# Performance work log

Hardware: AMD Instinct MI355X
Metric: run time of the kernel (lower is better)

Reference implementation:

```python
import jax, jax.numpy as jnp
import numpy as np
from jax import lax

# 4D convolution via lax.conv_general_dilated (supports N spatial dims natively)
# Layout: x is (N, C, T, U, V, W); weight is (O, I, kT, kU, kV, kW)

def conv4d(x, w, b):
    dn = lax.conv_dimension_numbers(x.shape, w.shape, ('NCTUVW', 'OITUVW', 'NCTUVW'))
    y = lax.conv_general_dilated(x, w, window_strides=(1, 1, 1, 1), padding='SAME',
                                 dimension_numbers=dn)
    return y + b[None, :, None, None, None, None]


def setup_inputs() -> dict:
    key = jax.random.key(0)
    k0, k1, k2, k3, k4 = jax.random.split(key, 5)
    B, C_in, C_hid, C_out = 2, 64, 128, 64
    T, D, H, W = 4, 16, 32, 32
    K = 3  # kernel size per dim (stmode 'C' -> (3,3,3,3))
    x = jax.random.normal(k0, (B, C_in, T, D, H, W), dtype=jnp.float32)
    scale1 = 1.0 / np.sqrt(C_in * K ** 4)
    scale2 = 1.0 / np.sqrt(C_hid * K ** 4)
    w1 = jax.random.normal(k1, (C_hid, C_in, K, K, K, K), dtype=jnp.float32) * scale1
    b1 = jax.random.normal(k2, (C_hid,), dtype=jnp.float32) * scale1
    w2 = jax.random.normal(k3, (C_out, C_hid, K, K, K, K), dtype=jnp.float32) * scale2
    b2 = jax.random.normal(k4, (C_out,), dtype=jnp.float32) * scale2
    return {"x": x, "w1": w1, "b1": b1, "w2": w2, "b2": b2}


def reference(x, w1, b1, w2, b2):
    # conv1 -> ReLU -> (dropout p=0 is identity) -> conv2 -> (dropout identity)
    h = jax.nn.relu(conv4d(x, w1, b1))
    return conv4d(h, w2, b2)
```

## Files before the change

kernel.cpp:

```cpp
#include <hip/hip_runtime.h>


using bf16x8 = __attribute__((ext_vector_type(8))) __bf16;
using f32x16 = __attribute__((ext_vector_type(16))) float;
using f32x4  = __attribute__((ext_vector_type(4))) float;

__global__ __launch_bounds__(256) void cvt_x(const float* __restrict__ x,
                                             __bf16* __restrict__ x_t) {
    __shared__ float lt[64][65];
    const int nb = blockIdx.y;
    const int p0 = blockIdx.x * 64;
    const float* src = x + (size_t)nb * 64 * 65536;
    __bf16* dst = x_t + (size_t)nb * 65536 * 64;
    #pragma unroll
    for (int i = 0; i < 16; ++i) {
        int idx = i * 256 + threadIdx.x;
        int c = idx >> 6, p = idx & 63;
        lt[c][p] = src[(size_t)c * 65536 + p0 + p];
    }
    __syncthreads();
    #pragma unroll
    for (int i = 0; i < 16; ++i) {
        int idx = i * 256 + threadIdx.x;
        int p = idx >> 6, c = idx & 63;
        dst[(size_t)(p0 + p) * 64 + c] = (__bf16)lt[c][p];
    }
}

template <int CIN>
__global__ __launch_bounds__(256) void cvt_w(const float* __restrict__ w,
                                             __bf16* __restrict__ wt) {
    constexpr int LOG = (CIN == 64) ? 6 : 7;
    constexpr int COUT = 8192 / CIN;
    int oc = blockIdx.x * 256 + threadIdx.x;
    if (oc >= 8192) return;
    const int o = oc >> LOG, c = oc & (CIN - 1);
    const int kg = c >> 4, cl = c & 15;
    const float* src = w + (size_t)oc * 81;
    #pragma unroll 1
    for (int tap = 0; tap < 81; ++tap)
        wt[(((size_t)tap * (CIN / 16) + kg) * COUT + o) * 16 + cl] = (__bf16)src[tap];
}

template <int CIN, int COUT, int MT, int NT, int CHALVES, bool RELU>
__global__ __launch_bounds__(256, 2) void conv4d_mfma(
    const __bf16* __restrict__ in_t,
    const __bf16* __restrict__ wt,
    const float* __restrict__ bias,
    __bf16* __restrict__ out_bf,
    float* __restrict__ out_f)
{
    __shared__ uint4 tile4[340 * 8];

    const int tid  = threadIdx.x;
    const int lane = tid & 63;
    const int l31  = lane & 31;
    const int hl   = lane >> 5;
    const int wv   = tid >> 6;
    const int gmi  = wv >> 1;
    const int gni  = wv & 1;

    const int bid = blockIdx.x;
    const int vg = bid & 3;
    const int u  = (bid >> 2) & 15;
    const int t  = (bid >> 6) & 3;
    const int nb = bid >> 8;
    const int v0 = vg * 8;
    const int pbase = ((t * 16 + u) * 32 + v0) * 32;

    const __bf16* inb = in_t + (size_t)nb * 65536 * CIN;

    f32x16 acc[MT][NT];
    #pragma unroll
    for (int mt = 0; mt < MT; ++mt)
        #pragma unroll
        for (int nt = 0; nt < NT; ++nt)
            #pragma unroll
            for (int i = 0; i < 16; ++i)
                acc[mt][nt][i] = 0.f;

    #pragma unroll 1
    for (int kt = 0; kt < 3; ++kt) {
        const int t_in = t + kt - 1;
        if ((unsigned)t_in >= 4u) continue;
        #pragma unroll 1
        for (int ku = 0; ku < 3; ++ku) {
            const int u_in = u + ku - 1;
            if ((unsigned)u_in >= 16u) continue;
            const int rowbase = (t_in * 16 + u_in) * 1024;
            #pragma unroll 1
            for (int ch = 0; ch < CHALVES; ++ch) {
                __syncthreads();
                #pragma unroll 1
                for (int idx = tid; idx < 2720; idx += 256) {
                    const int c = idx & 7, pos = idx >> 3;
                    const int r = pos / 34, wp = pos - r * 34;
                    const int v_in = v0 - 1 + r, w_in = wp - 1;
                    uint4 val = make_uint4(0u, 0u, 0u, 0u);
                    if (((unsigned)v_in < 32u) && ((unsigned)w_in < 32u))
                        val = *(const uint4*)(inb +
                              (size_t)(rowbase + v_in * 32 + w_in) * CIN +
                              ch * 64 + c * 8);
                    tile4[pos * 8 + (c ^ (pos & 7))] = val;
                }
                __syncthreads();
                const int tap00 = (kt * 3 + ku) * 3;
                #pragma unroll 1
                for (int kv = 0; kv < 3; ++kv) {
                    #pragma unroll
                    for (int kw = 0; kw < 3; ++kw) {
                        const int tap = (tap00 + kv) * 3 + kw;
                        const __bf16* bbase = wt +
                            ((size_t)tap * (CIN / 16) + ch * 4) * (COUT * 16);
                        #pragma unroll
                        for (int ks = 0; ks < 4; ++ks) {
                            bf16x8 af[MT];
                            #pragma unroll
                            for (int mt = 0; mt < MT; ++mt) {
                                const int pos = (gmi * MT + mt + kv) * 34 + l31 + kw;
                                af[mt] = *(const bf16x8*)&tile4[pos * 8 +
                                         ((ks * 2 + hl) ^ (pos & 7))];
                            }
                            bf16x8 bfv[NT];
                            #pragma unroll
                            for (int nt = 0; nt < NT; ++nt) {
                                const int o = (gni * NT + nt) * 32 + l31;
                                bfv[nt] = *(const bf16x8*)(bbase +
                                          (size_t)ks * (COUT * 16) + o * 16 + hl * 8);
                            }
                            #pragma unroll
                            for (int mt = 0; mt < MT; ++mt)
                                #pragma unroll
                                for (int nt = 0; nt < NT; ++nt)
                                    acc[mt][nt] = __builtin_amdgcn_mfma_f32_32x32x16_bf16(
                                        af[mt], bfv[nt], acc[mt][nt], 0, 0, 0);
                        }
                    }
                }
            }
        }
    }

    #pragma unroll
    for (int nt = 0; nt < NT; ++nt) {
        const int o = (gni * NT + nt) * 32 + l31;
        const float bv = bias[o];
        #pragma unroll
        for (int mt = 0; mt < MT; ++mt) {
            const int pb = pbase + (gmi * MT + mt) * 32;
            if constexpr (RELU) {
                #pragma unroll
                for (int rg = 0; rg < 4; ++rg)
                    #pragma unroll
                    for (int j = 0; j < 4; ++j) {
                        float v = acc[mt][nt][rg * 4 + j] + bv;
                        v = v > 0.f ? v : 0.f;
                        const int p = pb + j + 8 * rg + 4 * hl;
                        out_bf[(size_t)(nb * 65536 + p) * COUT + o] = (__bf16)v;
                    }
            } else {
                #pragma unroll
                for (int rg = 0; rg < 4; ++rg) {
                    f32x4 s;
                    #pragma unroll
                    for (int j = 0; j < 4; ++j)
                        s[j] = acc[mt][nt][rg * 4 + j] + bv;
                    const int p = pb + 8 * rg + 4 * hl;
                    *(f32x4*)(out_f + ((size_t)nb * COUT + o) * 65536 + p) = s;
                }
            }
        }
    }
}

extern "C" void kernel_launch(void* const* d_in, const int* in_sizes, int n_in,
                              void* d_out, int out_size, void* d_ws, size_t ws_size,
                              hipStream_t stream) {
    const float* x  = (const float*)d_in[0];
    const float* w1 = (const float*)d_in[1];
    const float* b1 = (const float*)d_in[2];
    const float* w2 = (const float*)d_in[3];
    const float* b2 = (const float*)d_in[4];
    float* out = (float*)d_out;

    char* ws = (char*)d_ws;
    __bf16* x_t = (__bf16*)ws;
    __bf16* h_t = (__bf16*)(ws + 16777216);
    __bf16* w1t = (__bf16*)(ws + 16777216 + 33554432);
    __bf16* w2t = (__bf16*)(ws + 16777216 + 33554432 + 1327104);

    cvt_x<<<dim3(1024, 2), 256, 0, stream>>>(x, x_t);
    cvt_w<64><<<32, 256, 0, stream>>>(w1, w1t);
    cvt_w<128><<<32, 256, 0, stream>>>(w2, w2t);

    conv4d_mfma<64, 128, 4, 2, 1, true><<<512, 256, 0, stream>>>(x_t, w1t, b1, h_t, nullptr);
    conv4d_mfma<128, 64, 4, 1, 2, false><<<512, 256, 0, stream>>>(h_t, w2t, b2, nullptr, out);
}
```

Measured before the change: 456.2 us.

## Stage input tiles with direct global-to-LDS loads and reuse A fragments across kv

```diff
diff --git a/kernel.cpp b/kernel.cpp
--- a/kernel.cpp
+++ b/kernel.cpp
@@ -4,6 +4,12 @@
 using bf16x8 = __attribute__((ext_vector_type(8))) __bf16;
 using f32x16 = __attribute__((ext_vector_type(16))) float;
 using f32x4  = __attribute__((ext_vector_type(4))) float;
+
+typedef __attribute__((address_space(1))) const void as1_void;
+typedef __attribute__((address_space(3))) void as3_void;
+__device__ __forceinline__ void gload_lds16(const void* g, void* l) {
+    __builtin_amdgcn_global_load_lds((as1_void*)g, (as3_void*)l, 16, 0, 0);
+}
 
 __global__ __launch_bounds__(256) void cvt_x(const float* __restrict__ x,
                                              __bf16* __restrict__ x_t) {
@@ -42,15 +48,17 @@
         wt[(((size_t)tap * (CIN / 16) + kg) * COUT + o) * 16 + cl] = (__bf16)src[tap];
 }
 
-template <int CIN, int COUT, int MT, int NT, int CHALVES, bool RELU>
+template <int CIN, int COUT, int NT, int CHALVES, bool RELU>
 __global__ __launch_bounds__(256, 2) void conv4d_mfma(
     const __bf16* __restrict__ in_t,
     const __bf16* __restrict__ wt,
     const float* __restrict__ bias,
     __bf16* __restrict__ out_bf,
-    float* __restrict__ out_f)
+    float* __restrict__ out_f,
+    const __bf16* __restrict__ zp)
 {
-    __shared__ uint4 tile4[340 * 8];
+    constexpr int KST = CIN / 16;
+    __shared__ __bf16 tile[3072 * 8];
 
     const int tid  = threadIdx.x;
     const int lane = tid & 63;
@@ -61,18 +69,45 @@
     const int gni  = wv & 1;
 
     const int bid = blockIdx.x;
-    const int vg = bid & 3;
-    const int u  = (bid >> 2) & 15;
-    const int t  = (bid >> 6) & 3;
-    const int nb = bid >> 8;
-    const int v0 = vg * 8;
+    const int xcd = bid & 7;
+    const int s   = bid >> 3;
+    const int u   = xcd * 2 + (s & 1);
+    const int vg  = (s >> 1) & 3;
+    const int t   = (s >> 3) & 3;
+    const int nb  = (s >> 5) & 1;
+    const int v0  = vg * 8;
     const int pbase = ((t * 16 + u) * 32 + v0) * 32;
 
     const __bf16* inb = in_t + (size_t)nb * 65536 * CIN;
 
-    f32x16 acc[MT][NT];
-    #pragma unroll
-    for (int mt = 0; mt < MT; ++mt)
+    int goff[12];
+    #pragma unroll
+    for (int it = 0; it < 12; ++it) {
+        const int idx = it * 256 + tid;
+        const int row = idx / 272;
+        const int rem = idx - row * 272;
+        const int chunk = rem / 34;
+        const int wp  = rem - chunk * 34;
+        const int v_in = v0 - 1 + row;
+        const int w_in = wp - 1;
+        const bool ok = (row < 10) && ((unsigned)v_in < 32u) && ((unsigned)w_in < 32u);
+        goff[it] = ok ? ((v_in * 32 + w_in) * CIN + chunk * 8) : -1;
+    }
+
+    const bf16x8* tile16 = (const bf16x8*)tile;
+    const bf16x8* abase[3];
+    #pragma unroll
+    for (int kw = 0; kw < 3; ++kw)
+        abase[kw] = tile16 + (gmi * 1088 + hl * 34 + l31 + kw);
+
+    const __bf16* wlane[NT];
+    #pragma unroll
+    for (int nt = 0; nt < NT; ++nt)
+        wlane[nt] = wt + ((gni * NT + nt) * 32 + l31) * 16 + hl * 8;
+
+    f32x16 acc[4][NT];
+    #pragma unroll
+    for (int mt = 0; mt < 4; ++mt)
         #pragma unroll
         for (int nt = 0; nt < NT; ++nt)
             #pragma unroll
@@ -87,55 +122,48 @@
         for (int ku = 0; ku < 3; ++ku) {
             const int u_in = u + ku - 1;
             if ((unsigned)u_in >= 16u) continue;
-            const int rowbase = (t_in * 16 + u_in) * 1024;
+            const int tapbase = (kt * 3 + ku) * 9;
+            const __bf16* gstage0 = inb + (size_t)((t_in * 16 + u_in) * 1024) * CIN;
             #pragma unroll 1
             for (int ch = 0; ch < CHALVES; ++ch) {
+                const __bf16* gstage = gstage0 + ch * 64;
                 __syncthreads();
-                #pragma unroll 1
-                for (int idx = tid; idx < 2720; idx += 256) {
-                    const int c = idx & 7, pos = idx >> 3;
-                    const int r = pos / 34, wp = pos - r * 34;
-                    const int v_in = v0 - 1 + r, w_in = wp - 1;
-                    uint4 val = make_uint4(0u, 0u, 0u, 0u);
-                    if (((unsigned)v_in < 32u) && ((unsigned)w_in < 32u))
-                        val = *(const uint4*)(inb +
-                              (size_t)(rowbase + v_in * 32 + w_in) * CIN +
-                              ch * 64 + c * 8);
-                    tile4[pos * 8 + (c ^ (pos & 7))] = val;
+                #pragma unroll
+                for (int it = 0; it < 12; ++it) {
+                    const __bf16* gp = (goff[it] >= 0) ? (gstage + goff[it]) : zp;
+                    char* lp = ((char*)tile) + it * 4096 + wv * 1024;
+                    gload_lds16(gp, lp);
                 }
                 __syncthreads();
-                const int tap00 = (kt * 3 + ku) * 3;
-                #pragma unroll 1
-                for (int kv = 0; kv < 3; ++kv) {
-                    #pragma unroll
-                    for (int kw = 0; kw < 3; ++kw) {
-                        const int tap = (tap00 + kv) * 3 + kw;
-                        const __bf16* bbase = wt +
-                            ((size_t)tap * (CIN / 16) + ch * 4) * (COUT * 16);
+                #pragma unroll
+                for (int ks = 0; ks < 4; ++ks) {
+                    const int ksg = ch * 4 + ks;
+                    bf16x8 af[6][3];
+                    #pragma unroll
+                    for (int r = 0; r < 6; ++r)
                         #pragma unroll
-                        for (int ks = 0; ks < 4; ++ks) {
-                            bf16x8 af[MT];
+                        for (int kw = 0; kw < 3; ++kw)
+                            af[r][kw] = abase[kw][r * 272 + ks * 68];
+                    #pragma unroll
+                    for (int kv = 0; kv < 3; ++kv)
+                        #pragma unroll
+                        for (int kw = 0; kw < 3; ++kw) {
+                            const size_t wo =
+                                ((size_t)(tapbase + kv * 3 + kw) * KST + ksg) *
+                                (COUT * 16);
+                            bf16x8 bv[NT];
                             #pragma unroll
-                            for (int mt = 0; mt < MT; ++mt) {
-                                const int pos = (gmi * MT + mt + kv) * 34 + l31 + kw;
-                                af[mt] = *(const bf16x8*)&tile4[pos * 8 +
-                                         ((ks * 2 + hl) ^ (pos & 7))];
-                            }
-                            bf16x8 bfv[NT];
+                            for (int nt = 0; nt < NT; ++nt)
+                                bv[nt] = *(const bf16x8*)(wlane[nt] + wo);
                             #pragma unroll
-                            for (int nt = 0; nt < NT; ++nt) {
-                                const int o = (gni * NT + nt) * 32 + l31;
-                                bfv[nt] = *(const bf16x8*)(bbase +
-                                          (size_t)ks * (COUT * 16) + o * 16 + hl * 8);
-                            }
-                            #pragma unroll
-                            for (int mt = 0; mt < MT; ++mt)
+                            for (int r = kv; r < kv + 4; ++r)
                                 #pragma unroll
                                 for (int nt = 0; nt < NT; ++nt)
-                                    acc[mt][nt] = __builtin_amdgcn_mfma_f32_32x32x16_bf16(
-                                        af[mt], bfv[nt], acc[mt][nt], 0, 0, 0);
+                                    acc[r - kv][nt] =
+                                        __builtin_amdgcn_mfma_f32_32x32x16_bf16(
+                                            af[r][kw], bv[nt], acc[r - kv][nt],
+                                            0, 0, 0);
                         }
-                    }
                 }
             }
         }
@@ -146,8 +174,8 @@
         const int o = (gni * NT + nt) * 32 + l31;
         const float bv = bias[o];
         #pragma unroll
-        for (int mt = 0; mt < MT; ++mt) {
-            const int pb = pbase + (gmi * MT + mt) * 32;
+        for (int mt = 0; mt < 4; ++mt) {
+            const int pb = pbase + (gmi * 4 + mt) * 32;
             if constexpr (RELU) {
                 #pragma unroll
                 for (int rg = 0; rg < 4; ++rg)
@@ -161,12 +189,12 @@
             } else {
                 #pragma unroll
                 for (int rg = 0; rg < 4; ++rg) {
-                    f32x4 s;
+                    f32x4 sv;
                     #pragma unroll
                     for (int j = 0; j < 4; ++j)
-                        s[j] = acc[mt][nt][rg * 4 + j] + bv;
+                        sv[j] = acc[mt][nt][rg * 4 + j] + bv;
                     const int p = pb + 8 * rg + 4 * hl;
-                    *(f32x4*)(out_f + ((size_t)nb * COUT + o) * 65536 + p) = s;
+                    *(f32x4*)(out_f + ((size_t)nb * COUT + o) * 65536 + p) = sv;
                 }
             }
         }
@@ -186,13 +214,17 @@
     char* ws = (char*)d_ws;
     __bf16* x_t = (__bf16*)ws;
     __bf16* h_t = (__bf16*)(ws + 16777216);
-    __bf16* w1t = (__bf16*)(ws + 16777216 + 33554432);
-    __bf16* w2t = (__bf16*)(ws + 16777216 + 33554432 + 1327104);
-
+    __bf16* w1t = (__bf16*)(ws + 50331648);
+    __bf16* w2t = (__bf16*)(ws + 51658752);
+    __bf16* zp  = (__bf16*)(ws + 52985856);
+
+    hipMemsetAsync(zp, 0, 256, stream);
     cvt_x<<<dim3(1024, 2), 256, 0, stream>>>(x, x_t);
     cvt_w<64><<<32, 256, 0, stream>>>(w1, w1t);
     cvt_w<128><<<32, 256, 0, stream>>>(w2, w2t);
 
-    conv4d_mfma<64, 128, 4, 2, 1, true><<<512, 256, 0, stream>>>(x_t, w1t, b1, h_t, nullptr);
-    conv4d_mfma<128, 64, 4, 1, 2, false><<<512, 256, 0, stream>>>(h_t, w2t, b2, nullptr, out);
-}
+    conv4d_mfma<64, 128, 2, 1, true><<<512, 256, 0, stream>>>(x_t, w1t, b1, h_t,
+                                                              nullptr, zp);
+    conv4d_mfma<128, 64, 1, 2, false><<<512, 256, 0, stream>>>(h_t, w2t, b2, nullptr,
+                                                               out, zp);
+}
```

New measurement: 402.8 us. -11.7%, faster.
